# Optimization experiments

Measured on AMD Instinct MI355X. Metric: run time of the kernel, lower is better.

The kernel has to match this reference:

```python
import jax, jax.numpy as jnp
import numpy as np

B, HT_, WT_, DM, C = 32, 32, 32, 768, 64  # batch, token grid, token dim, hough channels
THETA_RES, RHO_RES = 3, 1


def hough_transform(rows, cols, theta_res, rho_res):
    """Precompute binary vote matrix [rows*cols, n_rho*n_theta] (HT-LCNN style)."""
    theta = np.linspace(0.0, 180.0, int(np.ceil(180.0 / theta_res)) + 1)[:-1]
    w = theta.size                                # n_theta
    diag = np.sqrt((rows - 1) ** 2 + (cols - 1) ** 2)
    q = int(np.ceil(diag / rho_res))
    nrho = 2 * q + 1                              # n_rho
    cos_t, sin_t = np.cos(np.deg2rad(theta)), np.sin(np.deg2rad(theta))
    ii, jj = np.meshgrid(np.arange(rows), np.arange(cols), indexing='ij')
    xc = jj - cols / 2.0                          # centered pixel coords
    yc = rows / 2.0 - ii
    rho = xc[..., None] * cos_t + yc[..., None] * sin_t   # [rows, cols, w]
    ridx = np.round(rho / rho_res).astype(np.int64) + q
    tidx = np.broadcast_to(np.arange(w), ridx.shape)
    flat = (ridx * w + tidx).reshape(rows * cols, w)      # bin = rho_idx*w + theta_idx
    vote = np.zeros((rows * cols, nrho * w), dtype=np.float32)
    vote[np.arange(rows * cols)[:, None], flat] = 1.0
    return vote, nrho, w


def setup_inputs() -> dict:
    key = jax.random.key(0)
    ks = jax.random.split(key, 8)
    vote_np, n_rho, n_theta = hough_transform(HT_, WT_, THETA_RES, RHO_RES)
    ch = C // 2
    s = lambda n: 1.0 / np.sqrt(n)
    return dict(
        tokens=jax.random.normal(ks[0], (B, HT_ * WT_, DM), jnp.float32),
        vote=jnp.asarray(vote_np),                                    # [N, HR]
        Wt_in=jax.random.normal(ks[1], (C, DM), jnp.float32) * s(DM),   # to_feats 1x1
        bt_in=jnp.zeros((C,), jnp.float32),
        W1=jax.random.normal(ks[2], (ch, C), jnp.float32) * s(C),       # conv1 1x1 (no bias)
        W2=jax.random.normal(ks[3], (ch, ch, 9, 1), jnp.float32) * s(ch * 9),  # (9,1) conv on hough map
        W3=jax.random.normal(ks[4], (C, ch), jnp.float32) * s(ch),      # conv3 1x1 (no bias)
        Wt_out=jax.random.normal(ks[5], (DM, C), jnp.float32) * s(C),   # from_feats 1x1
        bt_out=jnp.zeros((DM,), jnp.float32),
        n_rho=n_rho,
        n_theta=n_theta,
    )


def reference(tokens, vote, Wt_in, bt_in, W1, W2, W3, Wt_out, bt_out, n_rho, n_theta):
    # tokens: [B, N, D]; vote: [N, HR] with HR = n_rho * n_theta.
    # 1x1 convs over the token grid are position-independent -> plain matmuls on [B, N, *].
    norm = jnp.clip(vote.sum(0), 1.0)                       # [HR] HT vote-count normalizer
    feat = tokens @ Wt_in.T + bt_in                         # [B, N, C]   (to_feats)
    y = jax.nn.relu(feat @ W1.T)                            # [B, N, ch]  (conv1 + relu)
    # HT: relu (idempotent here) + vote gather as dense matmul, normalized per hough bin
    ht = jnp.einsum('bnc,nh->bch', y, vote) / norm          # [B, ch, HR]
    bb, ch, hr = ht.shape
    ht = ht.reshape(bb, ch, n_rho, n_theta)                 # [B, ch, n_rho, n_theta]
    ht = jax.lax.conv_general_dilated(                      # (9,1) conv along rho, pad 4
        ht, W2, (1, 1), ((4, 4), (0, 0)),
        dimension_numbers=('NCHW', 'OIHW', 'NCHW'))
    # IHT: relu + transposed vote scatter, normalized by n_theta
    iht = jnp.einsum('bch,nh->bnc', jax.nn.relu(ht.reshape(bb, ch, hr)), vote) / n_theta
    z = iht @ W3.T                                          # [B, N, C]   (conv3)
    out = (feat + z) @ Wt_out.T + bt_out                    # residual + from_feats -> [B, N, D]
    return out
```

## Files before the change

### kernel.cpp

```cpp
#include <hip/hip_runtime.h>
#include <math.h>

#define NB    32
#define NTOK  1024
#define DMODEL 768
#define CF    64
#define CHH   32
#define NRHO  89
#define NTH   60
#define HRB   (NRHO*NTH)

typedef short bf16x8 __attribute__((ext_vector_type(8)));
typedef float f32x4  __attribute__((ext_vector_type(4)));
typedef unsigned int uint;
typedef unsigned short ushort;
typedef unsigned char uchar;

__device__ __forceinline__ ushort f2bf(float f) {
    uint u = __float_as_uint(f);
    return (ushort)((u + 0x7FFF + ((u >> 16) & 1)) >> 16);
}
__device__ __forceinline__ float bf2f(ushort u) {
    return __uint_as_float(((uint)u) << 16);
}
__device__ __forceinline__ uint cvtpk(float lo, float hi) {
    uint r;
    asm("v_cvt_pk_bf16_f32 %0, %1, %2" : "=v"(r) : "v"(lo), "v"(hi));
    return r;
}
__device__ __forceinline__ bf16x8 pack8(const float4& a, const float4& b) {
    uint4 u = make_uint4(cvtpk(a.x, a.y), cvtpk(a.z, a.w),
                         cvtpk(b.x, b.y), cvtpk(b.z, b.w));
    union { uint4 u4; bf16x8 v; } cv;
    cv.u4 = u;
    return cv.v;
}

__global__ __launch_bounds__(256) void k0_prep(
    int* __restrict__ perm, int* __restrict__ rowptr, uchar* __restrict__ rho8,
    const float* __restrict__ Wt_in, const float* __restrict__ bt_in,
    const float* __restrict__ W1, short* __restrict__ wcat,
    float* __restrict__ bcat,
    const float* __restrict__ Wt_out, const float* __restrict__ W2,
    short* __restrict__ wout, short* __restrict__ w2t) {
    __shared__ int rho_n[NTOK];
    __shared__ int cnt2[64 * 90];
    __shared__ int tot[96];
    __shared__ int base[96];
    __shared__ float w1row[64];
    const int tid = threadIdx.x;
    const int blk = blockIdx.x;

    if (blk < 60) {
        const int t = blk;
        const double rad = ((double)(t * 3)) * (M_PI / 180.0);
        const double ct = cos(rad), st = sin(rad);
        for (int n = tid; n < NTOK; n += 256) {
            int i = n >> 5, j = n & 31;
            double rho = (double)(j - 16) * ct + (double)(16 - i) * st;
            int ridx = (int)rint(rho) + 44;
            rho_n[n] = ridx;
            rho8[t * NTOK + n] = (uchar)ridx;
        }
        for (int i = tid; i < 64 * 90; i += 256) cnt2[i] = 0;
        __syncthreads();
        for (int n = tid; n < NTOK; n += 256)
            atomicAdd(&cnt2[(n >> 4) * 90 + rho_n[n]], 1);
        __syncthreads();
        if (tid < NRHO) {
            int s = 0;
            for (int c = 0; c < 64; ++c) {
                int v = cnt2[c * 90 + tid];
                cnt2[c * 90 + tid] = s;
                s += v;
            }
            tot[tid] = s;
        }
        __syncthreads();
        if (tid == 0) {
            int s = 0;
            for (int r = 0; r < NRHO; ++r) { base[r] = s; s += tot[r]; }
            base[NRHO] = s;
        }
        __syncthreads();
        if (tid < NRHO + 1) rowptr[t * 90 + tid] = base[tid];
        if (tid < 64) {
            const int c = tid;
            #pragma unroll
            for (int j = 0; j < 16; ++j) {
                int n = c * 16 + j;
                int r = rho_n[n];
                int cur = cnt2[c * 90 + r];
                cnt2[c * 90 + r] = cur + 1;
                perm[t * NTOK + base[r] + cur] = n;
            }
        }
    } else if (blk < 156) {
        const int c = blk - 60;
        if (c >= 64)
            for (int j = tid; j < 64; j += 256) w1row[j] = W1[(c - 64) * 64 + j];
        __syncthreads();
        for (int k = tid; k < DMODEL; k += 256) {
            float v;
            if (c < 64) v = Wt_in[c * DMODEL + k];
            else {
                v = 0.0f;
                for (int j = 0; j < 64; ++j) v += w1row[j] * Wt_in[j * DMODEL + k];
            }
            int kt = k >> 6, kk = k & 63;
            wcat[(((kt << 3) + (kk >> 3)) * 96 + c) * 8 + (k & 7)] = (short)f2bf(v);
        }
        if (tid == 0) {
            float bv;
            if (c < 64) bv = bt_in[c];
            else {
                bv = 0.0f;
                for (int j = 0; j < 64; ++j) bv += W1[(c - 64) * 64 + j] * bt_in[j];
            }
            bcat[c] = bv;
        }
    } else {
        int idx = (blk - 156) * 256 + tid;
        if (idx < 6144) {
            int d = idx >> 3, kg = idx & 7;
            float4 a = *(const float4*)&Wt_out[d * 64 + kg * 8];
            float4 b = *(const float4*)&Wt_out[d * 64 + kg * 8 + 4];
            uint4 v = make_uint4(cvtpk(a.x, a.y), cvtpk(a.z, a.w),
                                 cvtpk(b.x, b.y), cvtpk(b.z, b.w));
            *(uint4*)&wout[(((d >> 7) * 8 + kg) * 128 + (d & 127)) * 8] = v;
        } else if (idx < 6144 + 9216) {
            int q = idx - 6144;
            int e = q & 7, ln = (q >> 3) & 63, wm = (q >> 9) & 1, k = q >> 10;
            int o = wm * 16 + (ln & 15), i = ((ln >> 4) << 3) + e;
            w2t[q] = (short)f2bf(W2[(o * 32 + i) * 9 + k]);
        }
    }
}

__global__ __launch_bounds__(256, 4) void k1_mfma(
    const float* __restrict__ tokens, const short* __restrict__ wcat,
    const float* __restrict__ bcat, ushort* __restrict__ featb,
    ushort* __restrict__ ybb) {
    __shared__ ushort fs[32 * 64];
    __shared__ ushort ys[32 * 32];

    const int tid = threadIdx.x;
    const int lane = tid & 63, wave = tid >> 6;
    const int wm = wave >> 1, wn = wave & 1;
    const int row0 = blockIdx.x * 32;
    const int l15 = lane & 15, lq = lane >> 4;

    const float* aptr = tokens + (size_t)(row0 + wm * 16 + l15) * DMODEL + lq * 8;
    const short* bptr = wcat + ((size_t)lq * 96 + wn * 48 + l15) * 8;

    f32x4 acc[3] = {};

    float4 c0 = *(const float4*)&aptr[0],  c1 = *(const float4*)&aptr[4];
    float4 c2 = *(const float4*)&aptr[32], c3 = *(const float4*)&aptr[36];

    for (int kt = 0; kt < 12; ++kt) {
        float4 n0, n1, n2, n3;
        if (kt < 11) {
            const float* ap = aptr + (kt + 1) * 64;
            n0 = *(const float4*)&ap[0];  n1 = *(const float4*)&ap[4];
            n2 = *(const float4*)&ap[32]; n3 = *(const float4*)&ap[36];
        }
        bf16x8 a0 = pack8(c0, c1), a1 = pack8(c2, c3);
        const short* bp0 = bptr + (size_t)(kt * 8) * 96 * 8;
        const short* bp1 = bptr + (size_t)(kt * 8 + 4) * 96 * 8;
        bf16x8 b0 = *(const bf16x8*)&bp0[0];
        bf16x8 b1 = *(const bf16x8*)&bp0[16 * 8];
        bf16x8 b2 = *(const bf16x8*)&bp0[32 * 8];
        bf16x8 b3 = *(const bf16x8*)&bp1[0];
        bf16x8 b4 = *(const bf16x8*)&bp1[16 * 8];
        bf16x8 b5 = *(const bf16x8*)&bp1[32 * 8];
        acc[0] = __builtin_amdgcn_mfma_f32_16x16x32_bf16(a0, b0, acc[0], 0, 0, 0);
        acc[1] = __builtin_amdgcn_mfma_f32_16x16x32_bf16(a0, b1, acc[1], 0, 0, 0);
        acc[2] = __builtin_amdgcn_mfma_f32_16x16x32_bf16(a0, b2, acc[2], 0, 0, 0);
        acc[0] = __builtin_amdgcn_mfma_f32_16x16x32_bf16(a1, b3, acc[0], 0, 0, 0);
        acc[1] = __builtin_amdgcn_mfma_f32_16x16x32_bf16(a1, b4, acc[1], 0, 0, 0);
        acc[2] = __builtin_amdgcn_mfma_f32_16x16x32_bf16(a1, b5, acc[2], 0, 0, 0);
        c0 = n0; c1 = n1; c2 = n2; c3 = n3;
    }

    float bb[3];
    #pragma unroll
    for (int j = 0; j < 3; ++j) bb[j] = bcat[wn * 48 + j * 16 + l15];
    #pragma unroll
    for (int j = 0; j < 3; ++j) {
        int c = wn * 48 + j * 16 + l15;
        int mlb = wm * 16 + (lq << 2);
        #pragma unroll
        for (int r = 0; r < 4; ++r) {
            float v = acc[j][r] + bb[j];
            if (c < 64) fs[(mlb + r) * 64 + c] = f2bf(v);
            else        ys[(mlb + r) * 32 + (c - 64)] = f2bf(fmaxf(v, 0.0f));
        }
    }
    __syncthreads();
    if (tid < 256) {
        int ml = tid >> 3, cq = (tid & 7) * 8;
        *(uint4*)&featb[(size_t)(row0 + ml) * CF + cq] = *(const uint4*)&fs[ml * 64 + cq];
    }
    if (tid < 128) {
        int ml = tid >> 2, cq = (tid & 3) * 8;
        *(uint4*)&ybb[(size_t)(row0 + ml) * CHH + cq] = *(const uint4*)&ys[ml * 32 + cq];
    }
}

__global__ __launch_bounds__(256) void k23_ht_conv(
    const ushort* __restrict__ ybb, const int* __restrict__ perm,
    const int* __restrict__ rowptr, const short* __restrict__ w2t,
    ushort* __restrict__ htcT) {
    __shared__ int pperm[NTOK];
    __shared__ int prow[90];
    __shared__ __align__(16) short insp[104 * 40];
    __shared__ uint outtu[NRHO * 18];

    const int tid = threadIdx.x;
    const int lane = tid & 63, wave = tid >> 6;
    const int wm = wave >> 1, wn = wave & 1;
    const int b = blockIdx.x / NTH, t = blockIdx.x % NTH;

    bf16x8 av[9];
    #pragma unroll
    for (int k = 0; k < 9; ++k)
        av[k] = *(const bf16x8*)&w2t[(((k * 2 + wm) * 64) + lane) * 8];

    for (int i = tid; i < NTOK; i += 256) pperm[i] = perm[t * NTOK + i];
    for (int i = tid; i < 90; i += 256) prow[i] = rowptr[t * 90 + i];
    for (int i = tid; i < 104 * 40 / 2; i += 256) ((uint*)insp)[i] = 0;
    __syncthreads();

    {
        const int c0 = (tid & 3) * 8, g = tid >> 2;
        const ushort* yp = ybb + (size_t)b * NTOK * CHH + c0;
        for (int rho = g; rho < NRHO; rho += 64) {
            int p0 = prow[rho], p1 = prow[rho + 1];
            float s0 = 0, s1 = 0, s2 = 0, s3 = 0, s4 = 0, s5 = 0, s6 = 0, s7 = 0;
            for (int k = p0; k < p1; ++k) {
                int n = pperm[k];
                uint4 v = *(const uint4*)&yp[n * CHH];
                s0 += bf2f((ushort)(v.x & 0xffff)); s1 += bf2f((ushort)(v.x >> 16));
                s2 += bf2f((ushort)(v.y & 0xffff)); s3 += bf2f((ushort)(v.y >> 16));
                s4 += bf2f((ushort)(v.z & 0xffff)); s5 += bf2f((ushort)(v.z >> 16));
                s6 += bf2f((ushort)(v.w & 0xffff)); s7 += bf2f((ushort)(v.w >> 16));
            }
            float iv = 1.0f / fmaxf((float)(p1 - p0), 1.0f);
            uint4 pk = make_uint4(cvtpk(s0 * iv, s1 * iv), cvtpk(s2 * iv, s3 * iv),
                                  cvtpk(s4 * iv, s5 * iv), cvtpk(s6 * iv, s7 * iv));
            *(uint4*)&insp[(rho + 4) * 40 + c0] = pk;
        }
    }
    __syncthreads();

    f32x4 acc[3] = {};
    #pragma unroll
    for (int f = 0; f < 3; ++f) {
        int Rn = wn * 48 + f * 16 + (lane & 15);
        #pragma unroll
        for (int k = 0; k < 9; ++k) {
            bf16x8 bv = *(const bf16x8*)&insp[(Rn + k) * 40 + ((lane >> 4) << 3)];
            acc[f] = __builtin_amdgcn_mfma_f32_16x16x32_bf16(av[k], bv, acc[f], 0, 0, 0);
        }
    }
    #pragma unroll
    for (int f = 0; f < 3; ++f) {
        int r = wn * 48 + f * 16 + (lane & 15);
        if (r < NRHO) {
            int ob = wm * 8 + ((lane >> 4) << 1);
            outtu[r * 18 + ob]     = cvtpk(fmaxf(acc[f][0], 0.0f), fmaxf(acc[f][1], 0.0f));
            outtu[r * 18 + ob + 1] = cvtpk(fmaxf(acc[f][2], 0.0f), fmaxf(acc[f][3], 0.0f));
        }
    }
    __syncthreads();

    {
        ushort* dst = htcT + (size_t)(b * NTH + t) * (NRHO * CHH);
        for (int idx = tid; idx < NRHO * 8; idx += 256) {
            int r = idx >> 3, q = idx & 7;
            uint2 v;
            v.x = outtu[r * 18 + q * 2];
            v.y = outtu[r * 18 + q * 2 + 1];
            *(uint2*)&dst[r * CHH + q * 4] = v;
        }
    }
}

__global__ __launch_bounds__(256, 4) void k45_iht_out(
    const ushort* __restrict__ htcT, const uchar* __restrict__ rho8,
    const float* __restrict__ W3, const ushort* __restrict__ featb,
    const short* __restrict__ wout, const float* __restrict__ bt_out,
    float* __restrict__ out) {
    __shared__ float w3t[32 * 64];
    __shared__ uchar lrho[NTH * 64];
    __shared__ float ihts[64 * 32];
    __shared__ __align__(16) short Alds[4096];

    const int tid = threadIdx.x;
    const int lane = tid & 63, wave = tid >> 6;
    const int wm = wave >> 1, wn = wave & 1;
    const int bid = blockIdx.x;
    const int b = bid >> 4;
    const int n0 = (bid & 15) * 64;
    const int l15 = lane & 15, lq = lane >> 4;

    for (int idx = tid; idx < 2048; idx += 256) {
        int c = idx >> 6, j = idx & 63;
        w3t[idx] = W3[j * 32 + c];
    }
    for (int idx = tid; idx < NTH * 64; idx += 256)
        lrho[idx] = rho8[(idx >> 6) * NTOK + n0 + (idx & 63)];
    __syncthreads();

    {
        const int c0 = (tid & 3) * 8, tok = tid >> 2;
        const ushort* hb = htcT + (size_t)b * NTH * NRHO * CHH + c0;
        float s[8] = {};
        #pragma unroll 6
        for (int t = 0; t < NTH; ++t) {
            int r = lrho[t * 64 + tok];
            uint4 v = *(const uint4*)&hb[(size_t)(t * NRHO + r) * CHH];
            s[0] += bf2f((ushort)(v.x & 0xffff)); s[1] += bf2f((ushort)(v.x >> 16));
            s[2] += bf2f((ushort)(v.y & 0xffff)); s[3] += bf2f((ushort)(v.y >> 16));
            s[4] += bf2f((ushort)(v.z & 0xffff)); s[5] += bf2f((ushort)(v.z >> 16));
            s[6] += bf2f((ushort)(v.w & 0xffff)); s[7] += bf2f((ushort)(v.w >> 16));
        }
        float4 r0, r1;
        r0.x = s[0] * (1.0f / 60.0f); r0.y = s[1] * (1.0f / 60.0f);
        r0.z = s[2] * (1.0f / 60.0f); r0.w = s[3] * (1.0f / 60.0f);
        r1.x = s[4] * (1.0f / 60.0f); r1.y = s[5] * (1.0f / 60.0f);
        r1.z = s[6] * (1.0f / 60.0f); r1.w = s[7] * (1.0f / 60.0f);
        *(float4*)&ihts[tok * 32 + c0] = r0;
        *(float4*)&ihts[tok * 32 + c0 + 4] = r1;
    }
    __syncthreads();

    {
        const int j = tid & 63, nb = tid >> 6;
        ushort* Au = (ushort*)Alds;
        for (int nn = nb; nn < 64; nn += 4) {
            float z = 0.0f;
            #pragma unroll 8
            for (int cc = 0; cc < 32; ++cc) z += ihts[nn * 32 + cc] * w3t[cc * 64 + j];
            float v = bf2f(featb[(size_t)(bid * 64 + nn) * CF + j]) + z;
            Au[((j >> 3) * 64 + nn) * 8 + (j & 7)] = f2bf(v);
        }
    }
    __syncthreads();

    const bf16x8* Ap = (const bf16x8*)Alds;
    bf16x8 avr[2][2];
    #pragma unroll
    for (int ks = 0; ks < 2; ++ks) {
        int kg = lq + ks * 4;
        #pragma unroll
        for (int i = 0; i < 2; ++i)
            avr[ks][i] = Ap[kg * 64 + wm * 32 + i * 16 + l15];
    }

    const short* bbase = wout + ((size_t)lq * 128 + wn * 64 + l15) * 8;
    for (int db = 0; db < 6; ++db) {
        f32x4 acc[2][4] = {};
        #pragma unroll
        for (int ks = 0; ks < 2; ++ks) {
            const short* bp = bbase + ((size_t)(db * 8 + ks * 4) * 128) * 8;
            bf16x8 bvv[4];
            #pragma unroll
            for (int jf = 0; jf < 4; ++jf)
                bvv[jf] = *(const bf16x8*)&bp[jf * 16 * 8];
            #pragma unroll
            for (int i = 0; i < 2; ++i)
                #pragma unroll
                for (int jf = 0; jf < 4; ++jf)
                    acc[i][jf] = __builtin_amdgcn_mfma_f32_16x16x32_bf16(
                        avr[ks][i], bvv[jf], acc[i][jf], 0, 0, 0);
        }
        const int d0 = db * 128 + wn * 64 + l15;
        float bb[4];
        #pragma unroll
        for (int jf = 0; jf < 4; ++jf) bb[jf] = bt_out[d0 + jf * 16];
        const int mrow = bid * 64 + wm * 32 + (lq << 2);
        #pragma unroll
        for (int i = 0; i < 2; ++i)
            #pragma unroll
            for (int r = 0; r < 4; ++r)
                #pragma unroll
                for (int jf = 0; jf < 4; ++jf)
                    out[(size_t)(mrow + i * 16 + r) * DMODEL + d0 + jf * 16] =
                        acc[i][jf][r] + bb[jf];
    }
}

extern "C" void kernel_launch(void* const* d_in, const int* in_sizes, int n_in,
                              void* d_out, int out_size, void* d_ws, size_t ws_size,
                              hipStream_t stream) {
    const float* tokens = (const float*)d_in[0];
    const float* Wt_in  = (const float*)d_in[2];
    const float* bt_in  = (const float*)d_in[3];
    const float* W1     = (const float*)d_in[4];
    const float* W2     = (const float*)d_in[5];
    const float* W3     = (const float*)d_in[6];
    const float* Wt_out = (const float*)d_in[7];
    const float* bt_out = (const float*)d_in[8];
    float* out = (float*)d_out;

    char* w = (char*)d_ws;
    int*    perm   = (int*)(w);
    int*    rowptr = (int*)(w + 245760);
    uchar*  rho8   = (uchar*)(w + 267360);
    short*  wcat   = (short*)(w + 328800);
    float*  bcat   = (float*)(w + 476256);
    short*  wout   = (short*)(w + 476640);
    short*  w2t    = (short*)(w + 574944);
    ushort* featb  = (ushort*)(w + 593376);
    ushort* ybb    = (ushort*)(w + 4787680);
    ushort* htcT   = (ushort*)(w + 6884832);

    k0_prep<<<216, 256, 0, stream>>>(perm, rowptr, rho8, Wt_in, bt_in, W1,
                                     wcat, bcat, Wt_out, W2, wout, w2t);
    k1_mfma<<<NB * NTOK / 32, 256, 0, stream>>>(tokens, wcat, bcat, featb, ybb);
    k23_ht_conv<<<NB * NTH, 256, 0, stream>>>(ybb, perm, rowptr, w2t, htcT);
    k45_iht_out<<<NB * (NTOK / 64), 256, 0, stream>>>(htcT, rho8, W3, featb,
                                                      wout, bt_out, out);
}
```

Before: 113.7 us.

## Double-buffer output weights in LDS via async global-to-LDS loads

In the final from_feats GEMM kernel, the wout weight tiles are now staged into LDS with global_load_lds and double-buffered across the six output column blocks, so the next tile streams in while the current one feeds MFMAs. Shared memory is merged into one aliased buffer, which adds a barrier after the IHT gather loop and one per output block. A fragments are reloaded from LDS each iteration instead of being kept in registers. Separately, the first GEMM kernel issues its B loads before the prefetch of the next A tile and adds a sched_barrier to fix that ordering. The larger LDS footprint (40KB) and the extra barriers may reduce occupancy.

```diff
diff --git a/kernel.cpp b/kernel.cpp
--- a/kernel.cpp
+++ b/kernel.cpp
@@ -35,6 +35,10 @@
     cv.u4 = u;
     return cv.v;
 }
+
+#define GLDS16(gp, lp) __builtin_amdgcn_global_load_lds( \
+    (const __attribute__((address_space(1))) unsigned int*)(gp), \
+    (__attribute__((address_space(3))) unsigned int*)(lp), 16, 0, 0)
 
 __global__ __launch_bounds__(256) void k0_prep(
     int* __restrict__ perm, int* __restrict__ rowptr, uchar* __restrict__ rho8,
@@ -159,13 +163,6 @@
     float4 c2 = *(const float4*)&aptr[32], c3 = *(const float4*)&aptr[36];
 
     for (int kt = 0; kt < 12; ++kt) {
-        float4 n0, n1, n2, n3;
-        if (kt < 11) {
-            const float* ap = aptr + (kt + 1) * 64;
-            n0 = *(const float4*)&ap[0];  n1 = *(const float4*)&ap[4];
-            n2 = *(const float4*)&ap[32]; n3 = *(const float4*)&ap[36];
-        }
-        bf16x8 a0 = pack8(c0, c1), a1 = pack8(c2, c3);
         const short* bp0 = bptr + (size_t)(kt * 8) * 96 * 8;
         const short* bp1 = bptr + (size_t)(kt * 8 + 4) * 96 * 8;
         bf16x8 b0 = *(const bf16x8*)&bp0[0];
@@ -174,6 +171,15 @@
         bf16x8 b3 = *(const bf16x8*)&bp1[0];
         bf16x8 b4 = *(const bf16x8*)&bp1[16 * 8];
         bf16x8 b5 = *(const bf16x8*)&bp1[32 * 8];
+        float4 n0, n1, n2, n3;
+        if (kt < 11) {
+            const float* ap = aptr + (kt + 1) * 64;
+            n0 = *(const float4*)&ap[0];  n1 = *(const float4*)&ap[4];
+            n2 = *(const float4*)&ap[32]; n3 = *(const float4*)&ap[36];
+        }
+        __builtin_amdgcn_sched_barrier(0);
+
+        bf16x8 a0 = pack8(c0, c1), a1 = pack8(c2, c3);
         acc[0] = __builtin_amdgcn_mfma_f32_16x16x32_bf16(a0, b0, acc[0], 0, 0, 0);
         acc[1] = __builtin_amdgcn_mfma_f32_16x16x32_bf16(a0, b1, acc[1], 0, 0, 0);
         acc[2] = __builtin_amdgcn_mfma_f32_16x16x32_bf16(a0, b2, acc[2], 0, 0, 0);
@@ -292,10 +298,12 @@
     const float* __restrict__ W3, const ushort* __restrict__ featb,
     const short* __restrict__ wout, const float* __restrict__ bt_out,
     float* __restrict__ out) {
-    __shared__ float w3t[32 * 64];
-    __shared__ uchar lrho[NTH * 64];
-    __shared__ float ihts[64 * 32];
-    __shared__ __align__(16) short Alds[4096];
+    __shared__ __align__(16) char smem[40960];
+    short* Blds = (short*)smem;
+    short* Alds = (short*)(smem + 32768);
+    float* w3t  = (float*)smem;
+    uchar* lrho = (uchar*)(smem + 8192);
+    float* ihts = (float*)(smem + 12032);
 
     const int tid = threadIdx.x;
     const int lane = tid & 63, wave = tid >> 6;
@@ -303,7 +311,6 @@
     const int bid = blockIdx.x;
     const int b = bid >> 4;
     const int n0 = (bid & 15) * 64;
-    const int l15 = lane & 15, lq = lane >> 4;
 
     for (int idx = tid; idx < 2048; idx += 256) {
         int c = idx >> 6, j = idx & 63;
@@ -326,6 +333,7 @@
             s[4] += bf2f((ushort)(v.z & 0xffff)); s[5] += bf2f((ushort)(v.z >> 16));
             s[6] += bf2f((ushort)(v.w & 0xffff)); s[7] += bf2f((ushort)(v.w >> 16));
         }
+        __syncthreads();
         float4 r0, r1;
         r0.x = s[0] * (1.0f / 60.0f); r0.y = s[1] * (1.0f / 60.0f);
         r0.z = s[2] * (1.0f / 60.0f); r0.w = s[3] * (1.0f / 60.0f);
@@ -349,32 +357,37 @@
     }
     __syncthreads();
 
+    for (int ch = tid; ch < 1024; ch += 256)
+        GLDS16((const char*)wout + ch * 16, (char*)Blds + ch * 16);
+    __syncthreads();
+
     const bf16x8* Ap = (const bf16x8*)Alds;
-    bf16x8 avr[2][2];
-    #pragma unroll
-    for (int ks = 0; ks < 2; ++ks) {
-        int kg = lq + ks * 4;
-        #pragma unroll
-        for (int i = 0; i < 2; ++i)
-            avr[ks][i] = Ap[kg * 64 + wm * 32 + i * 16 + l15];
-    }
-
-    const short* bbase = wout + ((size_t)lq * 128 + wn * 64 + l15) * 8;
+    const int l15 = lane & 15, lq = lane >> 4;
     for (int db = 0; db < 6; ++db) {
+        if (db < 5) {
+            const char* src = (const char*)wout + (size_t)(db + 1) * 16384;
+            char* dst = (char*)Blds + ((db + 1) & 1) * 16384;
+            for (int ch = tid; ch < 1024; ch += 256)
+                GLDS16(src + ch * 16, dst + ch * 16);
+        }
+        const bf16x8* Bp = (const bf16x8*)((const char*)Blds + (db & 1) * 16384);
         f32x4 acc[2][4] = {};
         #pragma unroll
         for (int ks = 0; ks < 2; ++ks) {
-            const short* bp = bbase + ((size_t)(db * 8 + ks * 4) * 128) * 8;
-            bf16x8 bvv[4];
+            int kg = lq + ks * 4;
+            bf16x8 avv[2], bvv[4];
+            #pragma unroll
+            for (int i = 0; i < 2; ++i)
+                avv[i] = Ap[kg * 64 + wm * 32 + i * 16 + l15];
             #pragma unroll
             for (int jf = 0; jf < 4; ++jf)
-                bvv[jf] = *(const bf16x8*)&bp[jf * 16 * 8];
+                bvv[jf] = Bp[kg * 128 + wn * 64 + jf * 16 + l15];
             #pragma unroll
             for (int i = 0; i < 2; ++i)
                 #pragma unroll
                 for (int jf = 0; jf < 4; ++jf)
                     acc[i][jf] = __builtin_amdgcn_mfma_f32_16x16x32_bf16(
-                        avr[ks][i], bvv[jf], acc[i][jf], 0, 0, 0);
+                        avv[i], bvv[jf], acc[i][jf], 0, 0, 0);
         }
         const int d0 = db * 128 + wn * 64 + l15;
         float bb[4];
@@ -389,6 +402,7 @@
                 for (int jf = 0; jf < 4; ++jf)
                     out[(size_t)(mrow + i * 16 + r) * DMODEL + d0 + jf * 16] =
                         acc[i][jf][r] + bb[jf];
+        __syncthreads();
     }
 }
 
```

Measured after the change: 113.5 us. Within noise of the previous version (-0.2%).
